# Kernel tuning notes

Hardware: AMD Instinct MI355X
Metric: run time of the kernel (lower is better)

Reference implementation:

```python
import jax, jax.numpy as jnp
import numpy as np

HIDDEN = 1024
HEADS = 16
HEAD_DIM = HIDDEN // HEADS  # 64
MLP_HIDDEN = int(HIDDEN * 4.0)  # 4096
B, L = 2, 2048
EPS_LN = 1e-6
EPS_RMS = 1e-6


def setup_inputs() -> dict:
    key = jax.random.key(0)
    ks = jax.random.split(key, 12)
    s = 0.02
    return {
        "x": jax.random.normal(ks[0], (B, L, HIDDEN), jnp.float32),
        "vec": jax.random.normal(ks[1], (B, HIDDEN), jnp.float32),
        "pe": jax.random.normal(ks[2], (1, 1, L, HEAD_DIM // 2, 2, 2), jnp.float32),
        "w_mod": jax.random.normal(ks[3], (HIDDEN, 3 * HIDDEN), jnp.float32) * s,
        "b_mod": jnp.zeros((3 * HIDDEN,), jnp.float32),
        "w1": jax.random.normal(ks[4], (HIDDEN, 3 * HIDDEN + MLP_HIDDEN), jnp.float32) * s,
        "b1": jnp.zeros((3 * HIDDEN + MLP_HIDDEN,), jnp.float32),
        "w_mlp": jax.random.normal(ks[5], (MLP_HIDDEN, HIDDEN), jnp.float32) * s,
        "b_mlp": jnp.zeros((HIDDEN,), jnp.float32),
        "w2": jax.random.normal(ks[6], (2 * HIDDEN, HIDDEN), jnp.float32) * s,
        "b2": jnp.zeros((HIDDEN,), jnp.float32),
        "q_scale": jnp.ones((HEAD_DIM,), jnp.float32),
        "k_scale": jnp.ones((HEAD_DIM,), jnp.float32),
    }


def _layernorm(x, eps=EPS_LN):
    m = jnp.mean(x, axis=-1, keepdims=True)
    v = jnp.mean(jnp.square(x - m), axis=-1, keepdims=True)
    return (x - m) * jax.lax.rsqrt(v + eps)


def _rmsnorm(x, scale, eps=EPS_RMS):
    rrms = jax.lax.rsqrt(jnp.mean(jnp.square(x), axis=-1, keepdims=True) + eps)
    return x * rrms * scale


def _apply_rope(t, pe):
    # t: [B,H,L,D]; pe: [1,1,L,D//2,2,2]
    t_ = t.reshape(*t.shape[:-1], -1, 1, 2)  # [B,H,L,D//2,1,2]
    out = pe[..., 0] * t_[..., 0] + pe[..., 1] * t_[..., 1]  # [B,H,L,D//2,2]
    return out.reshape(t.shape)


def reference(x, vec, pe, w_mod, b_mod, w1, b1, w_mlp, b_mlp, w2, b2, q_scale, k_scale):
    # adaLN modulation: silu(vec) -> Dense(3*dim) -> shift, scale, gate
    mod = (jax.nn.silu(vec) @ w_mod + b_mod)[:, None, :]  # [B,1,3H]
    shift, scale, gate = jnp.split(mod, 3, axis=-1)
    x_mod = (1.0 + scale) * _layernorm(x) + shift
    # fused QKV + MLP projection
    h = x_mod @ w1 + b1  # [B,L,3H+MH]
    qkv, mlp = h[..., : 3 * HIDDEN], h[..., 3 * HIDDEN :]
    qkv = qkv.reshape(x.shape[0], x.shape[1], 3, HEADS, HEAD_DIM)
    qkv = jnp.transpose(qkv, (2, 0, 3, 1, 4))  # [3,B,H,L,D]
    q, k, v = qkv[0], qkv[1], qkv[2]
    # QK-RMSNorm per head-dim
    q = _rmsnorm(q, q_scale)
    k = _rmsnorm(k, k_scale)
    # RoPE
    q = _apply_rope(q, pe)
    k = _apply_rope(k, pe)
    # attention
    scores = jnp.einsum("bhqd,bhkd->bhqk", q, k) * (HEAD_DIM ** -0.5)
    probs = jax.nn.softmax(scores, axis=-1)
    attn = jnp.einsum("bhqk,bhkd->bhqd", probs, v)
    attn = jnp.transpose(attn, (0, 2, 1, 3)).reshape(x.shape[0], x.shape[1], HIDDEN)
    # mlp branch (Dense with tanh activation per source) + fused output proj
    mlp_out = jnp.tanh(mlp @ w_mlp + b_mlp)
    out = jnp.concatenate([attn, mlp_out], axis=-1) @ w2 + b2
    return x + gate * out
```

## Files before the change

kernel.cpp:

```cpp
#include <hip/hip_runtime.h>
#include <stdint.h>


#define HID  1024
#define NH   16
#define HD   64
#define MLP  4096
#define D1   7168
#define DQKV 3072
#define DCAT 2048
#define BB   2
#define LL   2048
#define TOK  4096

typedef __attribute__((ext_vector_type(8))) short    bf16x8;
typedef __attribute__((ext_vector_type(4))) float    f32x4;
typedef __attribute__((ext_vector_type(4))) unsigned int u32x4;

__device__ __forceinline__ float b2f(unsigned short u) {
    unsigned int v = ((unsigned int)u) << 16;
    float f; __builtin_memcpy(&f, &v, 4); return f;
}
__device__ __forceinline__ unsigned short f2b(float f) {
    unsigned int v; __builtin_memcpy(&v, &f, 4);
    unsigned int r = (v + 0x7FFFu + ((v >> 16) & 1u)) >> 16;
    return (unsigned short)r;
}
__device__ __forceinline__ unsigned int pkbf2(float a, float b) {
    unsigned int ua, ub;
    __builtin_memcpy(&ua, &a, 4); __builtin_memcpy(&ub, &b, 4);
    return ((ua + 0x8000u) >> 16) | ((ub + 0x8000u) & 0xFFFF0000u);
}
__device__ __forceinline__ unsigned int cvtpk(float a, float b) {
    unsigned int r;
    asm("v_cvt_pk_bf16_f32 %0, %1, %2" : "=v"(r) : "v"(a), "v"(b));
    return r;
}
__device__ __forceinline__ void gl_lds16(const unsigned short* g, unsigned short* l) {
    __builtin_amdgcn_global_load_lds(
        (const __attribute__((address_space(1))) unsigned int*)(g),
        (__attribute__((address_space(3))) unsigned int*)(l), 16, 0, 0);
}

__global__ void k_transpose3(const float* __restrict__ w1, unsigned short* __restrict__ w1T,
                             const float* __restrict__ wmlp, unsigned short* __restrict__ wmlpT,
                             const float* __restrict__ w2, unsigned short* __restrict__ w2T) {
    __shared__ float tile[32][33];
    int id = blockIdx.x;
    const float* in; unsigned short* out; int R, C, bx, by;
    if (id < 7168) {
        in = w1; out = w1T; R = 1024; C = 7168; bx = id % 224; by = id / 224;
    } else if (id < 11264) {
        int j = id - 7168; in = wmlp; out = wmlpT; R = 4096; C = 1024; bx = j & 31; by = j >> 5;
    } else {
        int j = id - 11264; in = w2; out = w2T; R = 2048; C = 1024; bx = j & 31; by = j >> 5;
    }
    int tx = threadIdx.x, ty = threadIdx.y;
    #pragma unroll
    for (int i = 0; i < 4; i++) {
        int r = by * 32 + ty + i * 8;
        int c = bx * 32 + tx;
        tile[ty + i * 8][tx] = in[(size_t)r * C + c];
    }
    __syncthreads();
    #pragma unroll
    for (int i = 0; i < 4; i++) {
        int ro = bx * 32 + ty + i * 8;
        int co = by * 32 + tx;
        out[(size_t)ro * R + co] = f2b(tile[tx][ty + i * 8]);
    }
}

__global__ void k_vtrans(const unsigned short* __restrict__ h,
                         unsigned short* __restrict__ vT) {
    __shared__ unsigned short tile[64][72];
    int bh = blockIdx.y;
    int b = bh >> 4, hh = bh & 15;
    int l0 = blockIdx.x * 64;
    int t = threadIdx.x;
    int r = t >> 2, c8 = (t & 3) * 16;
    const unsigned short* src = h + (size_t)b * LL * D1 + (size_t)(l0 + r) * D1
                                  + 2 * HID + hh * HD;
    u32x4 v0 = *(const u32x4*)(src + c8);
    u32x4 v1 = *(const u32x4*)(src + c8 + 8);
    *(u32x4*)(&tile[r][c8]) = v0;
    *(u32x4*)(&tile[r][c8 + 8]) = v1;
    __syncthreads();
    int od = t >> 2, k0 = (t & 3) * 16;
    unsigned short* dst = vT + ((size_t)bh * 64 + od) * LL + l0 + k0;
    u32x4 o0, o1;
    #pragma unroll
    for (int j = 0; j < 4; j++) {
        o0[j] = (unsigned int)tile[k0 + 2*j][od] | ((unsigned int)tile[k0 + 2*j + 1][od] << 16);
        o1[j] = (unsigned int)tile[k0 + 8 + 2*j][od] | ((unsigned int)tile[k0 + 9 + 2*j][od] << 16);
    }
    *(u32x4*)(dst) = o0;
    *(u32x4*)(dst + 8) = o1;
}

__global__ void k_mod(const float* __restrict__ vec,
                      const float* __restrict__ w_mod,
                      const float* __restrict__ b_mod,
                      float* __restrict__ mod) {
    __shared__ float sv[HID];
    __shared__ float red[8][32];
    int b = blockIdx.y, t = threadIdx.x;
    for (int j = t; j < HID; j += 256) {
        float v = vec[b * HID + j];
        sv[j] = v / (1.0f + __expf(-v));
    }
    __syncthreads();
    int n0 = blockIdx.x * 32;
    int on = t & 31, ks = t >> 5;
    float acc = 0.f;
    const float* wp = w_mod + (size_t)(ks * 128) * 3072 + n0 + on;
    #pragma unroll 4
    for (int k = 0; k < 128; k++) acc += sv[ks * 128 + k] * wp[(size_t)k * 3072];
    red[ks][on] = acc;
    __syncthreads();
    if (t < 32) {
        float s = 0.f;
        #pragma unroll
        for (int i = 0; i < 8; i++) s += red[i][t];
        mod[b * 3072 + n0 + t] = s + b_mod[n0 + t];
    }
}

__global__ void k_lnmod(const float* __restrict__ x,
                        const float* __restrict__ mod,
                        unsigned short* __restrict__ xmod) {
    int tok = blockIdx.x;
    int t = threadIdx.x;
    int b = tok >> 11;
    float4 v4 = *(const float4*)(x + (size_t)tok * HID + t * 4);
    float v0 = v4.x, v1 = v4.y, v2 = v4.z, v3 = v4.w;
    float s  = v0 + v1 + v2 + v3;
    float sq = v0*v0 + v1*v1 + v2*v2 + v3*v3;
    for (int off = 1; off < 64; off <<= 1) {
        s  += __shfl_xor(s,  off);
        sq += __shfl_xor(sq, off);
    }
    __shared__ float ls[4], lq[4];
    int w = t >> 6;
    if ((t & 63) == 0) { ls[w] = s; lq[w] = sq; }
    __syncthreads();
    s  = ls[0] + ls[1] + ls[2] + ls[3];
    sq = lq[0] + lq[1] + lq[2] + lq[3];
    float mean = s * (1.0f / HID);
    float var  = sq * (1.0f / HID) - mean * mean;
    float rstd = rsqrtf(var + 1e-6f);
    const float* mb = mod + b * 3072;
    float y[4] = {v0, v1, v2, v3};
    unsigned short r[4];
    #pragma unroll
    for (int j = 0; j < 4; j++) {
        int col = t * 4 + j;
        float nval = (y[j] - mean) * rstd;
        r[j] = f2b((1.0f + mb[1024 + col]) * nval + mb[col]);
    }
    unsigned int o0 = (unsigned int)r[0] | ((unsigned int)r[1] << 16);
    unsigned int o1 = (unsigned int)r[2] | ((unsigned int)r[3] << 16);
    *(uint2*)(xmod + (size_t)tok * HID + t * 4) = make_uint2(o0, o1);
}

template<int EPI>
__global__ __launch_bounds__(256) void k_gemm(
    const unsigned short* __restrict__ A, int lda,
    const unsigned short* __restrict__ Bt, int ldb,
    const float* __restrict__ bias,
    unsigned short* __restrict__ C, float* __restrict__ Cf, int ldc,
    int K,
    const float* __restrict__ xin,
    const float* __restrict__ mod) {
    __shared__ alignas(16) unsigned short As[128 * 64];
    __shared__ alignas(16) unsigned short Bs[128 * 64];
    int t = threadIdx.x;
    int bm = blockIdx.x, bn = blockIdx.y;
    int lane = t & 63, wave = t >> 6;
    int wm = (wave >> 1) * 64, wn = (wave & 1) * 64;
    int ln = lane & 15, kq = lane >> 4;
    int ln7 = ln & 7;

    f32x4 acc[4][4];
    #pragma unroll
    for (int i = 0; i < 4; i++)
        #pragma unroll
        for (int j = 0; j < 4; j++) acc[i][j] = {0.f, 0.f, 0.f, 0.f};

    int sr  = t >> 3;
    int scg = (t & 7) ^ (sr & 7);
    const unsigned short* Ab = A  + (size_t)(bm * 128) * lda;
    const unsigned short* Bb = Bt + (size_t)(bn * 128) * ldb;

    int ksplit = K / gridDim.z;
    int kbeg = blockIdx.z * ksplit, kend = kbeg + ksplit;

    for (int k0 = kbeg; k0 < kend; k0 += 64) {
        __syncthreads();
        #pragma unroll
        for (int c = 0; c < 4; c++) {
            gl_lds16(Ab + (size_t)(c * 32 + sr) * lda + k0 + scg * 8, &As[c * 2048 + t * 8]);
            gl_lds16(Bb + (size_t)(c * 32 + sr) * ldb + k0 + scg * 8, &Bs[c * 2048 + t * 8]);
        }
        __syncthreads();
        #pragma unroll
        for (int ks = 0; ks < 2; ks++) {
            int slot = ((ks * 4 + kq) ^ ln7) * 8;
            bf16x8 af[4], bfr[4];
            #pragma unroll
            for (int i = 0; i < 4; i++)
                af[i] = *(const bf16x8*)(&As[(wm + i * 16 + ln) * 64 + slot]);
            #pragma unroll
            for (int j = 0; j < 4; j++)
                bfr[j] = *(const bf16x8*)(&Bs[(wn + j * 16 + ln) * 64 + slot]);
            #pragma unroll
            for (int i = 0; i < 4; i++)
                #pragma unroll
                for (int j = 0; j < 4; j++)
                    acc[i][j] = __builtin_amdgcn_mfma_f32_16x16x32_bf16(af[i], bfr[j], acc[i][j], 0, 0, 0);
        }
    }

    #pragma unroll
    for (int i = 0; i < 4; i++) {
        #pragma unroll
        for (int j = 0; j < 4; j++) {
            int col = bn * 128 + wn + j * 16 + ln;
            float bv = (EPI == 3) ? 0.f : bias[col];
            #pragma unroll
            for (int r = 0; r < 4; r++) {
                int row = bm * 128 + wm + i * 16 + kq * 4 + r;
                float v = acc[i][j][r] + bv;
                if (EPI == 0) {
                    C[(size_t)row * ldc + col] = f2b(v);
                } else if (EPI == 1) {
                    C[(size_t)row * ldc + col] = f2b(tanhf(v));
                } else if (EPI == 2) {
                    int b = row >> 11;
                    Cf[(size_t)row * ldc + col] =
                        xin[(size_t)row * HID + col] + mod[b * 3072 + 2048 + col] * v;
                } else {
                    Cf[((size_t)blockIdx.z * TOK + row) * ldc + col] = v;
                }
            }
        }
    }
}

__global__ __launch_bounds__(256) void k_red1(const float* __restrict__ part,
                                              const float* __restrict__ bias,
                                              unsigned short* __restrict__ cat) {
    int idx = blockIdx.x * 256 + threadIdx.x;
    int row = idx >> 8;
    int c4  = (idx & 255) * 4;
    float4 p0 = *(const float4*)(part + (size_t)row * HID + c4);
    float4 p1 = *(const float4*)(part + ((size_t)TOK + row) * HID + c4);
    float4 bv = *(const float4*)(bias + c4);
    float a0 = tanhf(p0.x + p1.x + bv.x);
    float a1 = tanhf(p0.y + p1.y + bv.y);
    float a2 = tanhf(p0.z + p1.z + bv.z);
    float a3 = tanhf(p0.w + p1.w + bv.w);
    *(uint2*)(&cat[(size_t)row * DCAT + HID + c4]) =
        make_uint2(pkbf2(a0, a1), pkbf2(a2, a3));
}

__global__ __launch_bounds__(256) void k_red2(const float* __restrict__ part,
                                              const float* __restrict__ bias,
                                              const float* __restrict__ x,
                                              const float* __restrict__ mod,
                                              float* __restrict__ out) {
    int idx = blockIdx.x * 256 + threadIdx.x;
    int row = idx >> 8;
    int c4  = (idx & 255) * 4;
    int b = row >> 11;
    float4 p0 = *(const float4*)(part + (size_t)row * HID + c4);
    float4 p1 = *(const float4*)(part + ((size_t)TOK + row) * HID + c4);
    float4 bv = *(const float4*)(bias + c4);
    float4 gv = *(const float4*)(mod + b * 3072 + 2048 + c4);
    float4 xv = *(const float4*)(x + (size_t)row * HID + c4);
    float4 o;
    o.x = xv.x + gv.x * (p0.x + p1.x + bv.x);
    o.y = xv.y + gv.y * (p0.y + p1.y + bv.y);
    o.z = xv.z + gv.z * (p0.z + p1.z + bv.z);
    o.w = xv.w + gv.w * (p0.w + p1.w + bv.w);
    *(float4*)(out + (size_t)row * HID + c4) = o;
}

__global__ void k_qkrope(unsigned short* __restrict__ h,
                         const float* __restrict__ pe,
                         const float* __restrict__ q_scale,
                         const float* __restrict__ k_scale) {
    int tok = blockIdx.x;
    int l = tok & (LL - 1);
    int t = threadIdx.x;
    int lane = t & 63, wave = t >> 6;
    int hh = wave * 4 + (lane >> 4);
    int d0 = (lane & 15) * 4;
    unsigned short* row = h + (size_t)tok * D1;
    int i0 = d0 >> 1;
    const float* peb = pe + ((size_t)l * 32 + i0) * 4;
    float4 e0 = *(const float4*)(peb);
    float4 e1 = *(const float4*)(peb + 4);
    #pragma unroll
    for (int qk = 0; qk < 2; qk++) {
        unsigned short* p = row + qk * HID + hh * HD + d0;
        const float* sc = (qk == 0 ? q_scale : k_scale) + d0;
        uint2 qv = *(const uint2*)p;
        float v0 = b2f((unsigned short)(qv.x & 0xFFFF)), v1 = b2f((unsigned short)(qv.x >> 16));
        float v2 = b2f((unsigned short)(qv.y & 0xFFFF)), v3 = b2f((unsigned short)(qv.y >> 16));
        float ssq = v0*v0 + v1*v1 + v2*v2 + v3*v3;
        ssq += __shfl_xor(ssq, 1, 16);
        ssq += __shfl_xor(ssq, 2, 16);
        ssq += __shfl_xor(ssq, 4, 16);
        ssq += __shfl_xor(ssq, 8, 16);
        float rr = rsqrtf(ssq * (1.0f / HD) + 1e-6f);
        if (qk == 0) rr *= 0.18033688011112042f;
        v0 *= rr * sc[0];
        v1 *= rr * sc[1];
        v2 *= rr * sc[2];
        v3 *= rr * sc[3];
        float o0 = e0.x*v0 + e0.y*v1;
        float o1 = e0.z*v0 + e0.w*v1;
        float o2 = e1.x*v2 + e1.y*v3;
        float o3 = e1.z*v2 + e1.w*v3;
        *(uint2*)p = make_uint2(pkbf2(o0, o1), pkbf2(o2, o3));
    }
}

#define KT 64
__global__ __launch_bounds__(256) void k_attn(const unsigned short* __restrict__ h,
                                              const unsigned short* __restrict__ vT,
                                              unsigned short* __restrict__ cat) {
    __shared__ unsigned short Ks[KT * 64];
    __shared__ unsigned short Vt[HD * 64];
    __shared__ unsigned short Ps[4 * 16 * 64];
    int t = threadIdx.x;
    int bx = blockIdx.x;
    int bh = blockIdx.y;
    int b = bh >> 4, hh = bh & 15;
    int lane = t & 63, w = t >> 6;
    int ln = lane & 15, quad = lane >> 4;
    int ln7 = ln & 7;
    const unsigned short* hb = h + (size_t)b * LL * D1;

    int swk[2];
    swk[0] = ((0 + quad) ^ ln7) * 8;
    swk[1] = ((4 + quad) ^ ln7) * 8;

    bf16x8 qf[2];
    {
        const unsigned short* qbase = hb + (size_t)(bx * 64 + w * 16) * D1 + hh * HD;
        #pragma unroll
        for (int ks = 0; ks < 2; ks++)
            qf[ks] = *(const bf16x8*)(qbase + (size_t)ln * D1 + ks * 32 + quad * 8);
    }

    f32x4 O[4];
    #pragma unroll
    for (int vn = 0; vn < 4; vn++) O[vn] = {0.f, 0.f, 0.f, 0.f};
    float m_ = -1e30f, l_ = 0.f;

    unsigned short* Psw = Ps + w * 16 * 64;

    int skey = t >> 2, sdc16 = (t & 3) * 16, sc2 = (t & 3) * 2;
    const unsigned short* kbase0 = hb + HID + hh * HD;
    const unsigned short* vbase0 = vT + ((size_t)bh * 64 + skey) * LL;

    u32x4 ka = *(const u32x4*)(kbase0 + (size_t)skey * D1 + sdc16);
    u32x4 kc = *(const u32x4*)(kbase0 + (size_t)skey * D1 + sdc16 + 8);
    u32x4 va = *(const u32x4*)(vbase0 + sdc16);
    u32x4 vb = *(const u32x4*)(vbase0 + sdc16 + 8);

    for (int kb = 0; kb < LL / KT; kb++) {
        __syncthreads();
        {
            int k7 = skey & 7;
            *(u32x4*)(&Ks[skey * 64 + ((sc2 ^ k7) * 8)]) = ka;
            *(u32x4*)(&Ks[skey * 64 + (((sc2 + 1) ^ k7) * 8)]) = kc;
            *(u32x4*)(&Vt[skey * 64 + ((sc2 ^ k7) * 8)]) = va;
            *(u32x4*)(&Vt[skey * 64 + (((sc2 + 1) ^ k7) * 8)]) = vb;
        }
        __syncthreads();
        if (kb + 1 < LL / KT) {
            const unsigned short* kb1 = kbase0 + (size_t)(kb + 1) * KT * D1;
            const unsigned short* vb1 = vbase0 + (size_t)(kb + 1) * KT;
            ka = *(const u32x4*)(kb1 + (size_t)skey * D1 + sdc16);
            kc = *(const u32x4*)(kb1 + (size_t)skey * D1 + sdc16 + 8);
            va = *(const u32x4*)(vb1 + sdc16);
            vb = *(const u32x4*)(vb1 + sdc16 + 8);
        }

        f32x4 st[4];
        __builtin_amdgcn_s_setprio(1);
        #pragma unroll
        for (int kt = 0; kt < 4; kt++) {
            st[kt] = {0.f, 0.f, 0.f, 0.f};
            #pragma unroll
            for (int ks = 0; ks < 2; ks++) {
                bf16x8 kf = *(const bf16x8*)(&Ks[(kt * 16 + ln) * 64 + swk[ks]]);
                st[kt] = __builtin_amdgcn_mfma_f32_16x16x32_bf16(kf, qf[ks], st[kt], 0, 0, 0);
            }
        }
        __builtin_amdgcn_s_setprio(0);

        {
            float p[16];
            #pragma unroll
            for (int kt = 0; kt < 4; kt++)
                #pragma unroll
                for (int r = 0; r < 4; r++) p[kt * 4 + r] = st[kt][r];
            float a0 = fmaxf(fmaxf(p[0],  p[1]),  p[2]);
            float a1 = fmaxf(fmaxf(p[3],  p[4]),  p[5]);
            float a2 = fmaxf(fmaxf(p[6],  p[7]),  p[8]);
            float a3 = fmaxf(fmaxf(p[9],  p[10]), p[11]);
            float a4 = fmaxf(fmaxf(p[12], p[13]), p[14]);
            float mx = fmaxf(fmaxf(fmaxf(a0, a1), a2), fmaxf(fmaxf(a3, a4), p[15]));
            mx = fmaxf(mx, __shfl_xor(mx, 16));
            mx = fmaxf(mx, __shfl_xor(mx, 32));
            if (!__all(mx - m_ <= 10.f)) {
                float mnew = fmaxf(m_, mx);
                float alpha = __builtin_amdgcn_exp2f(m_ - mnew);
                m_ = mnew;
                l_ *= alpha;
                #pragma unroll
                for (int vn = 0; vn < 4; vn++)
                    #pragma unroll
                    for (int r = 0; r < 4; r++) O[vn][r] *= alpha;
            }
            #pragma unroll
            for (int i = 0; i < 16; i++) p[i] = __builtin_amdgcn_exp2f(p[i] - m_);
            float s0 = (p[0] + p[1]) + (p[2] + p[3]);
            float s1 = (p[4] + p[5]) + (p[6] + p[7]);
            float s2 = (p[8] + p[9]) + (p[10] + p[11]);
            float s3 = (p[12] + p[13]) + (p[14] + p[15]);
            float sum = (s0 + s1) + (s2 + s3);
            sum += __shfl_xor(sum, 16);
            sum += __shfl_xor(sum, 32);
            l_ += sum;
            #pragma unroll
            for (int kt = 0; kt < 4; kt++) {
                unsigned int w0 = cvtpk(p[kt*4+0], p[kt*4+1]);
                unsigned int w1 = cvtpk(p[kt*4+2], p[kt*4+3]);
                int pchunk = (2 * kt + (quad >> 1)) ^ ln7;
                *(uint2*)(&Psw[ln * 64 + pchunk * 8 + (quad & 1) * 4]) = make_uint2(w0, w1);
            }
        }

        __builtin_amdgcn_s_setprio(1);
        #pragma unroll
        for (int kt2 = 0; kt2 < 2; kt2++) {
            bf16x8 pb = *(const bf16x8*)(&Psw[ln * 64 + swk[kt2]]);
            #pragma unroll
            for (int vn = 0; vn < 4; vn++) {
                bf16x8 vf = *(const bf16x8*)(&Vt[(vn * 16 + ln) * 64 + swk[kt2]]);
                O[vn] = __builtin_amdgcn_mfma_f32_16x16x32_bf16(vf, pb, O[vn], 0, 0, 0);
            }
        }
        __builtin_amdgcn_s_setprio(0);
    }

    {
        float rl = 1.0f / l_;
        size_t row = (size_t)(b * LL + bx * 64 + w * 16 + ln);
        #pragma unroll
        for (int vn = 0; vn < 4; vn++) {
            #pragma unroll
            for (int r2 = 0; r2 < 4; r2 += 2) {
                unsigned int pk = cvtpk(O[vn][r2] * rl, O[vn][r2 + 1] * rl);
                *(unsigned int*)(&cat[row * DCAT + hh * HD + vn * 16 + quad * 4 + r2]) = pk;
            }
        }
    }
}

extern "C" void kernel_launch(void* const* d_in, const int* in_sizes, int n_in,
                              void* d_out, int out_size, void* d_ws, size_t ws_size,
                              hipStream_t stream) {
    const float* x       = (const float*)d_in[0];
    const float* vec     = (const float*)d_in[1];
    const float* pe      = (const float*)d_in[2];
    const float* w_mod   = (const float*)d_in[3];
    const float* b_mod   = (const float*)d_in[4];
    const float* w1      = (const float*)d_in[5];
    const float* b1      = (const float*)d_in[6];
    const float* w_mlp   = (const float*)d_in[7];
    const float* b_mlp   = (const float*)d_in[8];
    const float* w2      = (const float*)d_in[9];
    const float* b2      = (const float*)d_in[10];
    const float* q_scale = (const float*)d_in[11];
    const float* k_scale = (const float*)d_in[12];
    float* out = (float*)d_out;

    char* ws = (char*)d_ws;
    size_t off = 0;
    float* mod = (float*)(ws + off);                     off += 6144 * 4;
    unsigned short* xmod  = (unsigned short*)(ws + off); off += (size_t)TOK * HID * 2;
    unsigned short* h     = (unsigned short*)(ws + off); off += (size_t)TOK * D1 * 2;
    unsigned short* cat   = (unsigned short*)(ws + off); off += (size_t)TOK * DCAT * 2;
    unsigned short* w1T   = (unsigned short*)(ws + off); off += (size_t)D1 * HID * 2;
    unsigned short* wmlpT = (unsigned short*)(ws + off); off += (size_t)HID * MLP * 2;
    unsigned short* w2T   = (unsigned short*)(ws + off); off += (size_t)HID * DCAT * 2;
    float* part = (float*)(ws + off);                    off += (size_t)2 * TOK * HID * 4;
    unsigned short* vT    = (unsigned short*)(ws + off); off += (size_t)BB * NH * HD * LL * 2;

    k_transpose3<<<dim3(13312), dim3(32, 8), 0, stream>>>(w1, w1T, w_mlp, wmlpT, w2, w2T);

    k_mod<<<dim3(96, BB), 256, 0, stream>>>(vec, w_mod, b_mod, mod);
    k_lnmod<<<TOK, 256, 0, stream>>>(x, mod, xmod);

    k_gemm<0><<<dim3(TOK / 128, D1 / 128), 256, 0, stream>>>(
        xmod, HID, w1T, HID, b1, h, nullptr, D1, HID, nullptr, nullptr);

    k_qkrope<<<TOK, 256, 0, stream>>>(h, pe, q_scale, k_scale);
    k_vtrans<<<dim3(LL / 64, BB * NH), 256, 0, stream>>>(h, vT);

    k_attn<<<dim3(LL / 64, BB * NH), 256, 0, stream>>>(h, vT, cat);

    k_gemm<3><<<dim3(TOK / 128, HID / 128, 2), 256, 0, stream>>>(
        h + DQKV, D1, wmlpT, MLP, b_mlp, nullptr, part, HID, MLP, nullptr, nullptr);
    k_red1<<<TOK * HID / 1024, 256, 0, stream>>>(part, b_mlp, cat);

    k_gemm<3><<<dim3(TOK / 128, HID / 128, 2), 256, 0, stream>>>(
        cat, DCAT, w2T, DCAT, b2, nullptr, part, HID, DCAT, nullptr, nullptr);
    k_red2<<<TOK * HID / 1024, 256, 0, stream>>>(part, b2, x, mod, out);
}
```

Measured before the change: 405.7 us.

## Fuse V transpose into attention kernel and double query tile per block

Drops the separate V-transpose kernel and its workspace buffer. The attention kernel now loads V rows straight from the projection output and transposes them into swizzled shared memory while staging. Each block now handles 128 queries with 512 threads, so every K/V tile in shared memory is reused by twice as many query rows and a launch plus a global round trip are removed. In exchange, the scalar 16-bit repacking adds shared-memory stores per tile, and the larger blocks halve the grid size, which may lower occupancy.

After: 393.3 us. 3.1% less time.

```diff
diff --git a/kernel.cpp b/kernel.cpp
--- a/kernel.cpp
+++ b/kernel.cpp
@@ -69,33 +69,6 @@
         int co = by * 32 + tx;
         out[(size_t)ro * R + co] = f2b(tile[tx][ty + i * 8]);
     }
-}
-
-__global__ void k_vtrans(const unsigned short* __restrict__ h,
-                         unsigned short* __restrict__ vT) {
-    __shared__ unsigned short tile[64][72];
-    int bh = blockIdx.y;
-    int b = bh >> 4, hh = bh & 15;
-    int l0 = blockIdx.x * 64;
-    int t = threadIdx.x;
-    int r = t >> 2, c8 = (t & 3) * 16;
-    const unsigned short* src = h + (size_t)b * LL * D1 + (size_t)(l0 + r) * D1
-                                  + 2 * HID + hh * HD;
-    u32x4 v0 = *(const u32x4*)(src + c8);
-    u32x4 v1 = *(const u32x4*)(src + c8 + 8);
-    *(u32x4*)(&tile[r][c8]) = v0;
-    *(u32x4*)(&tile[r][c8 + 8]) = v1;
-    __syncthreads();
-    int od = t >> 2, k0 = (t & 3) * 16;
-    unsigned short* dst = vT + ((size_t)bh * 64 + od) * LL + l0 + k0;
-    u32x4 o0, o1;
-    #pragma unroll
-    for (int j = 0; j < 4; j++) {
-        o0[j] = (unsigned int)tile[k0 + 2*j][od] | ((unsigned int)tile[k0 + 2*j + 1][od] << 16);
-        o1[j] = (unsigned int)tile[k0 + 8 + 2*j][od] | ((unsigned int)tile[k0 + 9 + 2*j][od] << 16);
-    }
-    *(u32x4*)(dst) = o0;
-    *(u32x4*)(dst + 8) = o1;
 }
 
 __global__ void k_mod(const float* __restrict__ vec,
@@ -328,12 +301,11 @@
 }
 
 #define KT 64
-__global__ __launch_bounds__(256) void k_attn(const unsigned short* __restrict__ h,
-                                              const unsigned short* __restrict__ vT,
-                                              unsigned short* __restrict__ cat) {
+__global__ __launch_bounds__(512, 4) void k_attn(const unsigned short* __restrict__ h,
+                                                 unsigned short* __restrict__ cat) {
     __shared__ unsigned short Ks[KT * 64];
     __shared__ unsigned short Vt[HD * 64];
-    __shared__ unsigned short Ps[4 * 16 * 64];
+    __shared__ unsigned short Ps[8 * 16 * 64];
     int t = threadIdx.x;
     int bx = blockIdx.x;
     int bh = blockIdx.y;
@@ -349,7 +321,7 @@
 
     bf16x8 qf[2];
     {
-        const unsigned short* qbase = hb + (size_t)(bx * 64 + w * 16) * D1 + hh * HD;
+        const unsigned short* qbase = hb + (size_t)(bx * 128 + w * 16) * D1 + hh * HD;
         #pragma unroll
         for (int ks = 0; ks < 2; ks++)
             qf[ks] = *(const bf16x8*)(qbase + (size_t)ln * D1 + ks * 32 + quad * 8);
@@ -362,32 +334,36 @@
 
     unsigned short* Psw = Ps + w * 16 * 64;
 
-    int skey = t >> 2, sdc16 = (t & 3) * 16, sc2 = (t & 3) * 2;
+    int krow = t >> 3, kc = t & 7;
+    int kp2 = (t & 31) * 2, d0 = (t >> 5) * 4;
     const unsigned short* kbase0 = hb + HID + hh * HD;
-    const unsigned short* vbase0 = vT + ((size_t)bh * 64 + skey) * LL;
-
-    u32x4 ka = *(const u32x4*)(kbase0 + (size_t)skey * D1 + sdc16);
-    u32x4 kc = *(const u32x4*)(kbase0 + (size_t)skey * D1 + sdc16 + 8);
-    u32x4 va = *(const u32x4*)(vbase0 + sdc16);
-    u32x4 vb = *(const u32x4*)(vbase0 + sdc16 + 8);
+    const unsigned short* vbase0 = hb + 2 * HID + hh * HD;
+
+    u32x4 ka = *(const u32x4*)(kbase0 + (size_t)krow * D1 + kc * 8);
+    uint2  va = *(const uint2*)(vbase0 + (size_t)kp2 * D1 + d0);
+    uint2  vb = *(const uint2*)(vbase0 + (size_t)(kp2 + 1) * D1 + d0);
 
     for (int kb = 0; kb < LL / KT; kb++) {
         __syncthreads();
         {
-            int k7 = skey & 7;
-            *(u32x4*)(&Ks[skey * 64 + ((sc2 ^ k7) * 8)]) = ka;
-            *(u32x4*)(&Ks[skey * 64 + (((sc2 + 1) ^ k7) * 8)]) = kc;
-            *(u32x4*)(&Vt[skey * 64 + ((sc2 ^ k7) * 8)]) = va;
-            *(u32x4*)(&Vt[skey * 64 + (((sc2 + 1) ^ k7) * 8)]) = vb;
+            *(u32x4*)(&Ks[krow * 64 + ((kc ^ (krow & 7)) * 8)]) = ka;
+            #pragma unroll
+            for (int j = 0; j < 4; j++) {
+                unsigned int aw = (j < 2) ? va.x : va.y;
+                unsigned int bw = (j < 2) ? vb.x : vb.y;
+                unsigned int lo = (j & 1) ? (aw >> 16) : (aw & 0xFFFFu);
+                unsigned int hi = (j & 1) ? (bw >> 16) : (bw & 0xFFFFu);
+                int d = d0 + j;
+                *(unsigned int*)(&Vt[d * 64 + (kp2 ^ ((d & 7) << 3))]) = lo | (hi << 16);
+            }
         }
         __syncthreads();
         if (kb + 1 < LL / KT) {
             const unsigned short* kb1 = kbase0 + (size_t)(kb + 1) * KT * D1;
-            const unsigned short* vb1 = vbase0 + (size_t)(kb + 1) * KT;
-            ka = *(const u32x4*)(kb1 + (size_t)skey * D1 + sdc16);
-            kc = *(const u32x4*)(kb1 + (size_t)skey * D1 + sdc16 + 8);
-            va = *(const u32x4*)(vb1 + sdc16);
-            vb = *(const u32x4*)(vb1 + sdc16 + 8);
+            const unsigned short* vb1 = vbase0 + (size_t)(kb + 1) * KT * D1;
+            ka = *(const u32x4*)(kb1 + (size_t)krow * D1 + kc * 8);
+            va = *(const uint2*)(vb1 + (size_t)kp2 * D1 + d0);
+            vb = *(const uint2*)(vb1 + (size_t)(kp2 + 1) * D1 + d0);
         }
 
         f32x4 st[4];
@@ -461,7 +437,7 @@
 
     {
         float rl = 1.0f / l_;
-        size_t row = (size_t)(b * LL + bx * 64 + w * 16 + ln);
+        size_t row = (size_t)(b * LL + bx * 128 + w * 16 + ln);
         #pragma unroll
         for (int vn = 0; vn < 4; vn++) {
             #pragma unroll
@@ -501,7 +477,6 @@
     unsigned short* wmlpT = (unsigned short*)(ws + off); off += (size_t)HID * MLP * 2;
     unsigned short* w2T   = (unsigned short*)(ws + off); off += (size_t)HID * DCAT * 2;
     float* part = (float*)(ws + off);                    off += (size_t)2 * TOK * HID * 4;
-    unsigned short* vT    = (unsigned short*)(ws + off); off += (size_t)BB * NH * HD * LL * 2;
 
     k_transpose3<<<dim3(13312), dim3(32, 8), 0, stream>>>(w1, w1T, w_mlp, wmlpT, w2, w2T);
 
@@ -512,9 +487,8 @@
         xmod, HID, w1T, HID, b1, h, nullptr, D1, HID, nullptr, nullptr);
 
     k_qkrope<<<TOK, 256, 0, stream>>>(h, pe, q_scale, k_scale);
-    k_vtrans<<<dim3(LL / 64, BB * NH), 256, 0, stream>>>(h, vT);
-
-    k_attn<<<dim3(LL / 64, BB * NH), 256, 0, stream>>>(h, vT, cat);
+
+    k_attn<<<dim3(LL / 128, BB * NH), 512, 0, stream>>>(h, cat);
 
     k_gemm<3><<<dim3(TOK / 128, HID / 128, 2), 256, 0, stream>>>(
         h + DQKV, D1, wmlpT, MLP, b_mlp, nullptr, part, HID, MLP, nullptr, nullptr);
```
